# Optimization experiments

Hardware: AMD Instinct MI355X
Metric: run time of the kernel (lower is better)

## Reference

```python
import jax, jax.numpy as jnp
import numpy as np

N = 100_000
E = 1_600_000
C_IN, C_HID, C_OUT = 128, 128, 64


def setup_inputs() -> dict:
    key = jax.random.key(0)
    ks = jax.random.split(key, 10)
    inp = {
        "x": jax.random.normal(ks[0], (N, C_IN), dtype=jnp.float32),
        "edge_index": jax.random.randint(ks[1], (2, E), 0, N, dtype=jnp.int64),
        "edge_weight": jax.random.uniform(ks[2], (E,), dtype=jnp.float32),
        # learned params: 2 hidden GCN layers + output GCN layer (glorot-ish scale)
        "W1": jax.random.normal(ks[3], (C_IN, C_HID), dtype=jnp.float32) / np.sqrt(C_IN),
        "b1": jnp.zeros((C_HID,), dtype=jnp.float32),
        "W2": jax.random.normal(ks[4], (C_HID, C_HID), dtype=jnp.float32) / np.sqrt(C_HID),
        "b2": jnp.zeros((C_HID,), dtype=jnp.float32),
        "W3": jax.random.normal(ks[5], (C_HID, C_OUT), dtype=jnp.float32) / np.sqrt(C_HID),
        "b3": jnp.zeros((C_OUT,), dtype=jnp.float32),
    }
    return inp


def _gcn_conv(x, src, dst, w, W, b):
    # PyG GCNConv: h = X @ W; out[j] = sum_{(i->j)} norm_ij * h[i] + b
    # norm_ij = deg_i^{-1/2} * w_ij * deg_j^{-1/2}, deg = weighted in-degree (incl. self loops)
    h = x @ W                                      # [N, out]
    deg = jax.ops.segment_sum(w, dst, num_segments=N)  # [N]
    dinv = jnp.where(deg > 0, jax.lax.rsqrt(deg), 0.0)
    norm = dinv[src] * w * dinv[dst]               # [E']
    msg = h[src] * norm[:, None]                   # [E', out] gather-scale
    out = jax.ops.segment_sum(msg, dst, num_segments=N)  # scatter-add
    return out + b


def reference(x, edge_index, edge_weight, W1, b1, W2, b2, W3, b3):
    # add self loops once (weight 1.0), as GCNConv does per layer
    loop = jnp.arange(N, dtype=edge_index.dtype)
    src = jnp.concatenate([edge_index[0], loop])
    dst = jnp.concatenate([edge_index[1], loop])
    w = jnp.concatenate([edge_weight, jnp.ones((N,), dtype=edge_weight.dtype)])

    h = _gcn_conv(x, src, dst, w, W1, b1)
    h = jax.nn.relu(h)          # Dropout is identity in eval mode
    h = _gcn_conv(h, src, dst, w, W2, b2)
    h = jax.nn.relu(h)
    out = _gcn_conv(h, src, dst, w, W3, b3)
    return out
```

## Files before the change

### kernel.cpp

```cpp
#include <hip/hip_runtime.h>
#include <cstdint>
#include <cstddef>

#define TPB 256
#define PKS 16

__device__ __forceinline__ unsigned short f2bf(float f) {
  unsigned u = __float_as_uint(f);
  u += 0x7fffu + ((u >> 16) & 1u);
  return (unsigned short)(u >> 16);
}
__device__ __forceinline__ float bf_lo(unsigned u) { return __uint_as_float(u << 16); }
__device__ __forceinline__ float bf_hi(unsigned u) { return __uint_as_float(u & 0xffff0000u); }

#define FIXP 262144.0f
#define LOWMASK 0xFFFFFFFFFFULL

typedef __attribute__((ext_vector_type(8))) short  short8v;
typedef __attribute__((ext_vector_type(4))) float  float4v;


__global__ void init_k(unsigned long long* __restrict__ pk, int n) {
  int i = blockIdx.x * TPB + threadIdx.x;
  if (i < n * PKS) pk[i] = 0ULL;
}

__global__ void edges_k(const int* __restrict__ ei, const float* __restrict__ w,
                        unsigned long long* __restrict__ pk, int* __restrict__ pir, int E) {
  int e = blockIdx.x * TPB + threadIdx.x;
  if (e >= E) return;
  int d = ei[E + e];
  unsigned long long v = (1ULL << 40) | (unsigned long long)(w[e] * FIXP + 0.5f);
  unsigned long long old = atomicAdd(&pk[(size_t)d * PKS], v);
  pir[e] = (int)(old >> 40);
}

__global__ void unpack_k(const unsigned long long* __restrict__ pk,
                         float* __restrict__ dinv, int* __restrict__ cnt, int n) {
  int i = blockIdx.x * TPB + threadIdx.x;
  if (i >= n) return;
  unsigned long long p = pk[(size_t)i * PKS];
  float deg = 1.0f + (float)(p & LOWMASK) * (1.0f / FIXP);
  dinv[i] = rsqrtf(deg);
  cnt[i]  = (int)(p >> 40);
}

__global__ void scan_a(const int* __restrict__ cnt, int* __restrict__ rp,
                       int* __restrict__ bsum, int n) {
  __shared__ int s[TPB];
  int i = blockIdx.x * TPB + threadIdx.x;
  int v = (i < n) ? cnt[i] : 0;
  s[threadIdx.x] = v;
  __syncthreads();
  #pragma unroll
  for (int off = 1; off < TPB; off <<= 1) {
    int t = (threadIdx.x >= off) ? s[threadIdx.x - off] : 0;
    __syncthreads();
    s[threadIdx.x] += t;
    __syncthreads();
  }
  if (i < n) rp[i] = s[threadIdx.x] - v;
  if (threadIdx.x == TPB - 1) bsum[blockIdx.x] = s[TPB - 1];
}

__global__ void scan_b(int* __restrict__ bsum, int nb) {
  __shared__ int s[512];
  int v = (threadIdx.x < nb) ? bsum[threadIdx.x] : 0;
  s[threadIdx.x] = v;
  __syncthreads();
  #pragma unroll
  for (int off = 1; off < 512; off <<= 1) {
    int t = (threadIdx.x >= off) ? s[threadIdx.x - off] : 0;
    __syncthreads();
    s[threadIdx.x] += t;
    __syncthreads();
  }
  if (threadIdx.x < nb) bsum[threadIdx.x] = s[threadIdx.x] - v;
}

__global__ void scan_c(int* __restrict__ rp, const int* __restrict__ bsum, int n, int etot) {
  int i = blockIdx.x * TPB + threadIdx.x;
  if (i < n) rp[i] += bsum[blockIdx.x];
  if (blockIdx.x == 0 && threadIdx.x == 0) rp[n] = etot;
}

__global__ void fill_k(const int* __restrict__ ei, const float* __restrict__ w,
                       const float* __restrict__ dinv, const int* __restrict__ rp,
                       const int* __restrict__ pir, int2* __restrict__ epk, int E) {
  int e = blockIdx.x * TPB + threadIdx.x;
  if (e >= E) return;
  int s = ei[e];
  int d = ei[E + e];
  int pos = rp[d] + pir[e];
  float nrm = dinv[s] * w[e] * dinv[d];
  epk[pos] = make_int2(s, __float_as_int(nrm));
}

__global__ void wt_k(const float* __restrict__ W1, const float* __restrict__ W2,
                     const float* __restrict__ W3,
                     unsigned short* __restrict__ wt1, unsigned short* __restrict__ wt2,
                     unsigned short* __restrict__ wt3) {
  int t = blockIdx.x * TPB + threadIdx.x;
  if (t < 16384) {
    int c = t >> 7, k = t & 127;
    wt1[t] = f2bf(W1[k * 128 + c]);
  } else if (t < 32768) {
    int u = t - 16384;
    int c = u >> 7, k = u & 127;
    wt2[u] = f2bf(W2[k * 128 + c]);
  } else if (t < 40960) {
    int u = t - 32768;
    int c = u >> 7, k = u & 127;
    wt3[u] = f2bf(W3[k * 64 + c]);
  }
}


template<int COUT, bool RELU>
__global__ __launch_bounds__(256) void gemm_mfma(const float* __restrict__ X,
                                                 const unsigned short* __restrict__ Wt,
                                                 unsigned short* __restrict__ H, int n) {
  const int lane = threadIdx.x & 63;
  const int wv   = threadIdx.x >> 6;
  const int r0   = (blockIdx.x * 4 + wv) * 16;
  if (r0 >= n) return;
  const int c16   = lane & 15;
  const int kb    = (lane >> 4) * 8;
  const int row_c = min(r0 + c16, n - 1);

  short8v a[4];
  const float* xrow = X + (size_t)row_c * 128;
  #pragma unroll
  for (int kk = 0; kk < 4; kk++) {
    float4 lo = *(const float4*)(xrow + kk * 32 + kb);
    float4 hi = *(const float4*)(xrow + kk * 32 + kb + 4);
    float v0 = lo.x, v1 = lo.y, v2 = lo.z, v3 = lo.w;
    float v4 = hi.x, v5 = hi.y, v6 = hi.z, v7 = hi.w;
    if (RELU) {
      v0 = fmaxf(v0, 0.f); v1 = fmaxf(v1, 0.f); v2 = fmaxf(v2, 0.f); v3 = fmaxf(v3, 0.f);
      v4 = fmaxf(v4, 0.f); v5 = fmaxf(v5, 0.f); v6 = fmaxf(v6, 0.f); v7 = fmaxf(v7, 0.f);
    }
    short8v t;
    t[0] = (short)f2bf(v0); t[1] = (short)f2bf(v1);
    t[2] = (short)f2bf(v2); t[3] = (short)f2bf(v3);
    t[4] = (short)f2bf(v4); t[5] = (short)f2bf(v5);
    t[6] = (short)f2bf(v6); t[7] = (short)f2bf(v7);
    a[kk] = t;
  }

  constexpr int CT = COUT / 16;
  const int orow = r0 + (lane >> 4) * 4;
  #pragma unroll
  for (int ct = 0; ct < CT; ct++) {
    float4v acc = {0.f, 0.f, 0.f, 0.f};
    const unsigned short* wrow = Wt + (size_t)(ct * 16 + c16) * 128 + kb;
    #pragma unroll
    for (int kk = 0; kk < 4; kk++) {
      short8v b = *(const short8v*)(wrow + kk * 32);
      acc = __builtin_amdgcn_mfma_f32_16x16x32_bf16(a[kk], b, acc, 0, 0, 0);
    }
    const int ocol = ct * 16 + c16;
    #pragma unroll
    for (int r = 0; r < 4; r++) {
      if (orow + r < n)
        H[(size_t)(orow + r) * COUT + ocol] = f2bf(acc[r]);
    }
  }
}


__global__ __launch_bounds__(256) void agg128(const unsigned short* __restrict__ H,
                                              const int* __restrict__ rp,
                                              const int2* __restrict__ epk,
                                              const float* __restrict__ dinv,
                                              const float* __restrict__ bias,
                                              float* __restrict__ OUT, int n) {
  int wid  = __builtin_amdgcn_readfirstlane(blockIdx.x * 4 + (threadIdx.x >> 6));
  int lane = threadIdx.x & 63;
  if (wid >= n) return;
  float di = dinv[wid];
  float w0 = di * di;
  unsigned hv = ((const unsigned*)(H + (size_t)wid * 128))[lane];
  float2 bv = ((const float2*)bias)[lane];
  float ax = bv.x + w0 * bf_lo(hv);
  float ay = bv.y + w0 * bf_hi(hv);
  int e  = rp[wid];
  int e1 = rp[wid + 1];
  for (; e + 7 < e1; e += 8) {
    int2 p[8];
    #pragma unroll
    for (int u = 0; u < 8; u++) p[u] = epk[e + u];
    unsigned h[8];
    #pragma unroll
    for (int u = 0; u < 8; u++) h[u] = ((const unsigned*)(H + (size_t)p[u].x * 128))[lane];
    #pragma unroll
    for (int u = 0; u < 8; u++) {
      float nw = __int_as_float(p[u].y);
      ax += nw * bf_lo(h[u]);
      ay += nw * bf_hi(h[u]);
    }
  }
  for (; e < e1; e++) {
    int2 p = epk[e];
    unsigned h = ((const unsigned*)(H + (size_t)p.x * 128))[lane];
    float nw = __int_as_float(p.y);
    ax += nw * bf_lo(h); ay += nw * bf_hi(h);
  }
  ((float2*)(OUT + (size_t)wid * 128))[lane] = make_float2(ax, ay);
}

__global__ __launch_bounds__(256) void agg64(const unsigned short* __restrict__ H,
                                             const int* __restrict__ rp,
                                             const int2* __restrict__ epk,
                                             const float* __restrict__ dinv,
                                             const float* __restrict__ bias,
                                             float* __restrict__ OUT, int n) {
  int wid  = __builtin_amdgcn_readfirstlane(blockIdx.x * 4 + (threadIdx.x >> 6));
  int lane = threadIdx.x & 63;
  if (wid >= n) return;
  float di = dinv[wid];
  float w0 = di * di;
  float hv = __uint_as_float(((unsigned)H[(size_t)wid * 64 + lane]) << 16);
  float acc = bias[lane] + w0 * hv;
  int e  = rp[wid];
  int e1 = rp[wid + 1];
  for (; e + 7 < e1; e += 8) {
    int2 p[8];
    #pragma unroll
    for (int u = 0; u < 8; u++) p[u] = epk[e + u];
    float h[8];
    #pragma unroll
    for (int u = 0; u < 8; u++)
      h[u] = __uint_as_float(((unsigned)H[(size_t)p[u].x * 64 + lane]) << 16);
    #pragma unroll
    for (int u = 0; u < 8; u++) acc += __int_as_float(p[u].y) * h[u];
  }
  for (; e < e1; e++) {
    int2 p = epk[e];
    float h = __uint_as_float(((unsigned)H[(size_t)p.x * 64 + lane]) << 16);
    acc += __int_as_float(p.y) * h;
  }
  OUT[(size_t)wid * 64 + lane] = acc;
}


extern "C" void kernel_launch(void* const* d_in, const int* in_sizes, int n_in,
                              void* d_out, int out_size, void* d_ws, size_t ws_size,
                              hipStream_t stream) {
  const float* x  = (const float*)d_in[0];
  const int*   ei = (const int*)d_in[1];
  const float* ew = (const float*)d_in[2];
  const float* W1 = (const float*)d_in[3];
  const float* b1 = (const float*)d_in[4];
  const float* W2 = (const float*)d_in[5];
  const float* b2 = (const float*)d_in[6];
  const float* W3 = (const float*)d_in[7];
  const float* b3 = (const float*)d_in[8];

  const int N = in_sizes[0] / 128;
  const int E = in_sizes[2];

  char* p = (char*)d_ws;
  auto carve = [&](size_t bytes) -> void* {
    void* r = (void*)p;
    p += (bytes + 255) & ~(size_t)255;
    return r;
  };
  unsigned long long* pk = (unsigned long long*)carve((size_t)N * 8 * PKS);
  float* dinv   = (float*)carve((size_t)N * 4);
  int*   cnt    = (int*)  carve((size_t)N * 4);
  int*   rp     = (int*)  carve((size_t)(N + 1) * 4);
  int*   bsum   = (int*)  carve(512 * 4);
  int*   pir    = (int*)  carve((size_t)E * 4);
  int2*  epk    = (int2*) carve((size_t)E * 8);
  unsigned short* hbuf = (unsigned short*)carve((size_t)N * 128 * 2);
  float* abuf   = (float*)carve((size_t)N * 128 * 4);
  unsigned short* wt1 = (unsigned short*)carve(16384 * 2);
  unsigned short* wt2 = (unsigned short*)carve(16384 * 2);
  unsigned short* wt3 = (unsigned short*)carve(8192 * 2);

  const int NB = (N + TPB - 1) / TPB;
  const int EB = (E + TPB - 1) / TPB;

  init_k<<<(N * PKS + TPB - 1) / TPB, TPB, 0, stream>>>(pk, N);
  edges_k<<<EB, TPB, 0, stream>>>(ei, ew, pk, pir, E);
  unpack_k<<<NB, TPB, 0, stream>>>(pk, dinv, cnt, N);
  scan_a<<<NB, TPB, 0, stream>>>(cnt, rp, bsum, N);
  scan_b<<<1, 512, 0, stream>>>(bsum, NB);
  scan_c<<<NB, TPB, 0, stream>>>(rp, bsum, N, E);
  fill_k<<<EB, TPB, 0, stream>>>(ei, ew, dinv, rp, pir, epk, E);
  wt_k<<<160, TPB, 0, stream>>>(W1, W2, W3, wt1, wt2, wt3);

  const int aggBlocks  = (N + 3) / 4;
  const int gemmBlocks = (N + 63) / 64;

  gemm_mfma<128, false><<<gemmBlocks, 256, 0, stream>>>(x, wt1, hbuf, N);
  agg128<<<aggBlocks, 256, 0, stream>>>(hbuf, rp, epk, dinv, b1, abuf, N);

  gemm_mfma<128, true><<<gemmBlocks, 256, 0, stream>>>(abuf, wt2, hbuf, N);
  agg128<<<aggBlocks, 256, 0, stream>>>(hbuf, rp, epk, dinv, b2, abuf, N);

  gemm_mfma<64, true><<<gemmBlocks, 256, 0, stream>>>(abuf, wt3, hbuf, N);
  agg64<<<aggBlocks, 256, 0, stream>>>(hbuf, rp, epk, dinv, b3, (float*)d_out, N);
}
```

Baseline: 395.0 us.

## Sort CSR rows by source, vectorize edge loads, use nontemporal loads and stores

```diff
diff --git a/kernel.cpp b/kernel.cpp
--- a/kernel.cpp
+++ b/kernel.cpp
@@ -18,6 +18,7 @@
 
 typedef __attribute__((ext_vector_type(8))) short  short8v;
 typedef __attribute__((ext_vector_type(4))) float  float4v;
+typedef __attribute__((ext_vector_type(4))) int    int4v;
 
 
 __global__ void init_k(unsigned long long* __restrict__ pk, int n) {
@@ -94,6 +95,34 @@
   int pos = rp[d] + pir[e];
   float nrm = dinv[s] * w[e] * dinv[d];
   epk[pos] = make_int2(s, __float_as_int(nrm));
+}
+
+__global__ __launch_bounds__(256) void sort_rows(int2* __restrict__ epk,
+                                                 const int* __restrict__ rp, int n) {
+  int wid  = blockIdx.x * 4 + (threadIdx.x >> 6);
+  int lane = threadIdx.x & 63;
+  if (wid >= n) return;
+  int e0 = rp[wid], e1 = rp[wid + 1];
+  int deg = e1 - e0;
+  if (deg <= 1 || deg > 64) return;
+  unsigned long long val = ~0ULL;
+  if (lane < deg) {
+    int2 p = epk[e0 + lane];
+    val = ((unsigned long long)(unsigned)p.x << 32) | (unsigned)p.y;
+  }
+  #pragma unroll
+  for (int k = 2; k <= 64; k <<= 1) {
+    #pragma unroll
+    for (int j = k >> 1; j >= 1; j >>= 1) {
+      unsigned long long o = __shfl_xor(val, j, 64);
+      bool takeMin = (((lane & j) == 0) == ((lane & k) == 0));
+      unsigned long long mn = val < o ? val : o;
+      unsigned long long mx = val < o ? o : val;
+      val = takeMin ? mn : mx;
+    }
+  }
+  if (lane < deg)
+    epk[e0 + lane] = make_int2((int)(val >> 32), (int)(unsigned)(val & 0xffffffffu));
 }
 
 __global__ void wt_k(const float* __restrict__ W1, const float* __restrict__ W2,
@@ -186,18 +215,29 @@
   float ay = bv.y + w0 * bf_hi(hv);
   int e  = rp[wid];
   int e1 = rp[wid + 1];
+  if ((e & 1) && e < e1) {
+    int2 p = epk[e];
+    unsigned h = ((const unsigned*)(H + (size_t)p.x * 128))[lane];
+    float nw = __int_as_float(p.y);
+    ax += nw * bf_lo(h); ay += nw * bf_hi(h);
+    e++;
+  }
+  const int4v* ep4 = (const int4v*)epk;
   for (; e + 7 < e1; e += 8) {
-    int2 p[8];
-    #pragma unroll
-    for (int u = 0; u < 8; u++) p[u] = epk[e + u];
+    int4v q[4];
+    #pragma unroll
+    for (int u = 0; u < 4; u++) q[u] = __builtin_nontemporal_load(&ep4[(e >> 1) + u]);
     unsigned h[8];
     #pragma unroll
-    for (int u = 0; u < 8; u++) h[u] = ((const unsigned*)(H + (size_t)p[u].x * 128))[lane];
-    #pragma unroll
-    for (int u = 0; u < 8; u++) {
-      float nw = __int_as_float(p[u].y);
-      ax += nw * bf_lo(h[u]);
-      ay += nw * bf_hi(h[u]);
+    for (int u = 0; u < 4; u++) {
+      h[2*u]   = ((const unsigned*)(H + (size_t)q[u][0] * 128))[lane];
+      h[2*u+1] = ((const unsigned*)(H + (size_t)q[u][2] * 128))[lane];
+    }
+    #pragma unroll
+    for (int u = 0; u < 4; u++) {
+      float n0 = __int_as_float(q[u][1]), n1 = __int_as_float(q[u][3]);
+      ax += n0 * bf_lo(h[2*u]);   ay += n0 * bf_hi(h[2*u]);
+      ax += n1 * bf_lo(h[2*u+1]); ay += n1 * bf_hi(h[2*u+1]);
     }
   }
   for (; e < e1; e++) {
@@ -206,7 +246,9 @@
     float nw = __int_as_float(p.y);
     ax += nw * bf_lo(h); ay += nw * bf_hi(h);
   }
-  ((float2*)(OUT + (size_t)wid * 128))[lane] = make_float2(ax, ay);
+  float2 o = make_float2(ax, ay);
+  __builtin_nontemporal_store(*(const double*)&o,
+                              (double*)(OUT + (size_t)wid * 128) + lane);
 }
 
 __global__ __launch_bounds__(256) void agg64(const unsigned short* __restrict__ H,
@@ -224,23 +266,35 @@
   float acc = bias[lane] + w0 * hv;
   int e  = rp[wid];
   int e1 = rp[wid + 1];
+  if ((e & 1) && e < e1) {
+    int2 p = epk[e];
+    float h = __uint_as_float(((unsigned)H[(size_t)p.x * 64 + lane]) << 16);
+    acc += __int_as_float(p.y) * h;
+    e++;
+  }
+  const int4v* ep4 = (const int4v*)epk;
   for (; e + 7 < e1; e += 8) {
-    int2 p[8];
-    #pragma unroll
-    for (int u = 0; u < 8; u++) p[u] = epk[e + u];
+    int4v q[4];
+    #pragma unroll
+    for (int u = 0; u < 4; u++) q[u] = __builtin_nontemporal_load(&ep4[(e >> 1) + u]);
     float h[8];
     #pragma unroll
-    for (int u = 0; u < 8; u++)
-      h[u] = __uint_as_float(((unsigned)H[(size_t)p[u].x * 64 + lane]) << 16);
-    #pragma unroll
-    for (int u = 0; u < 8; u++) acc += __int_as_float(p[u].y) * h[u];
+    for (int u = 0; u < 4; u++) {
+      h[2*u]   = __uint_as_float(((unsigned)H[(size_t)q[u][0] * 64 + lane]) << 16);
+      h[2*u+1] = __uint_as_float(((unsigned)H[(size_t)q[u][2] * 64 + lane]) << 16);
+    }
+    #pragma unroll
+    for (int u = 0; u < 4; u++) {
+      acc += __int_as_float(q[u][1]) * h[2*u];
+      acc += __int_as_float(q[u][3]) * h[2*u+1];
+    }
   }
   for (; e < e1; e++) {
     int2 p = epk[e];
     float h = __uint_as_float(((unsigned)H[(size_t)p.x * 64 + lane]) << 16);
     acc += __int_as_float(p.y) * h;
   }
-  OUT[(size_t)wid * 64 + lane] = acc;
+  __builtin_nontemporal_store(acc, OUT + (size_t)wid * 64 + lane);
 }
 
 
@@ -294,6 +348,8 @@
   const int aggBlocks  = (N + 3) / 4;
   const int gemmBlocks = (N + 63) / 64;
 
+  sort_rows<<<aggBlocks, 256, 0, stream>>>(epk, rp, N);
+
   gemm_mfma<128, false><<<gemmBlocks, 256, 0, stream>>>(x, wt1, hbuf, N);
   agg128<<<aggBlocks, 256, 0, stream>>>(hbuf, rp, epk, dinv, b1, abuf, N);
 
```

New measurement: 451.0 us. 1.14x slower.
